# Optimization experiments

Hardware: AMD Instinct MI355X
Metric: run time of the kernel (lower is better)

The kernel has to match this reference:

```python
import jax, jax.numpy as jnp
import numpy as np

B, N, C, T = 2048, 512, 64, 128  # batch, codebook size, latent channels, latent time


def setup_inputs() -> dict:
    key = jax.random.key(0)
    k1, k2 = jax.random.split(key)
    y = jax.random.normal(k1, (B, C, T), dtype=jnp.float32)   # encoder latents
    m = jax.random.normal(k2, (N, C, T), dtype=jnp.float32)   # centroid means
    sd = jnp.ones((N, C, T), dtype=jnp.float32)               # centroid variances
    p = jnp.zeros((N,), dtype=jnp.float32) + 1e-6             # cluster counts
    return {"y": y, "m": m, "sd": sd, "p": p}


def reference(y, m, sd, p):
    # --- squared-distance argmin assignment (same math as (y-m)^2 summed over C,T) ---
    b = y.shape[0]
    yf = y.reshape(b, -1)                 # [B, D]
    mf = m.reshape(m.shape[0], -1)        # [N, D]
    d2 = (yf * yf).sum(-1)[:, None] + (mf * mf).sum(-1)[None, :] - 2.0 * (yf @ mf.T)
    assign = jnp.argmin(d2, axis=1)       # [B] int assignments

    # --- sequential, order-sensitive EMA scatter updates (faithful to python loop) ---
    def step(carry, inp):
        p_, m_, sd_ = carry
        yi, zi = inp
        p_ = p_.at[zi].add(1.0)
        mi = m_[zi] * 0.001 + yi * 0.999
        m_ = m_.at[zi].set(mi)
        sdi = (mi - yi) ** 2 * 0.001 + sd_[zi] * 0.999
        sd_ = sd_.at[zi].set(sdi)
        return (p_, m_, sd_), None

    (p, m, sd), _ = jax.lax.scan(step, (p, m, sd), (y, assign))
    return m, sd, p, assign
```

## Files before the change

kernel.cpp:

```cpp
#include <hip/hip_runtime.h>
#include <hip/hip_bf16.h>


#define Bb 2048
#define Nn 512
#define Dd 8192
#define MARGIN 12.0f
#define KC 8
#define KSTEPS 32

typedef __attribute__((ext_vector_type(4))) float f32x4;
typedef __attribute__((ext_vector_type(8))) short s16x8;

union Frag { unsigned u[4]; s16x8 s; };

__device__ inline unsigned pack2(float lo, float hi) {
    return __builtin_amdgcn_perm(__float_as_uint(hi), __float_as_uint(lo), 0x07060302u);
}

__device__ inline void ema4(float4& mcv, float4& scv, const float4 yv) {
#define EMA_C(c) { mcv.c = mcv.c * 0.001f + yv.c * 0.999f; \
                   float d_ = mcv.c - yv.c;                 \
                   scv.c = d_ * d_ * 0.001f + scv.c * 0.999f; }
    EMA_C(x) EMA_C(y) EMA_C(z) EMA_C(w)
#undef EMA_C
}

__global__ __launch_bounds__(256) void m_norms(const float* __restrict__ M,
                                               float* __restrict__ mm) {
    int n = blockIdx.x, t = threadIdx.x;
    const float4* r = (const float4*)(M + (size_t)n * Dd);
    float s = 0.f;
#pragma unroll
    for (int u = 0; u < 8; u++) {
        float4 v = r[t + 256 * u];
        s += v.x * v.x + v.y * v.y + v.z * v.z + v.w * v.w;
    }
    __shared__ float red[256];
    red[t] = s;
    __syncthreads();
    for (int off = 128; off > 0; off >>= 1) {
        if (t < off) red[t] += red[t + off];
        __syncthreads();
    }
    if (t == 0) mm[n] = red[0];
}

__global__ __launch_bounds__(512, 4) void gemm_coarse(const float* __restrict__ Y,
                                                      const float* __restrict__ M,
                                                      float* __restrict__ part) {
    __shared__ __align__(16) float As[2][128 * 32];
    __shared__ __align__(16) float Bs[2][128 * 32];
    const int t = threadIdx.x;
    const int lane = t & 63;
    const int w = t >> 6;

    const int bid = blockIdx.x;
    const int kc = bid & 7;
    const int ct = (bid >> 3) & 3;
    const int rt = bid >> 5;

    const size_t ybase = (size_t)rt * 128 * Dd + (size_t)kc * (KSTEPS * 32);
    const size_t mbase = (size_t)ct * 128 * Dd + (size_t)kc * (KSTEPS * 32);

    int rowS[2], soff[2];
#pragma unroll
    for (int u = 0; u < 2; u++) {
        int flat = (w * 2 + u) * 64 + lane;
        int row = flat >> 3, seg = flat & 7;
        rowS[u] = row;
        soff[u] = (seg ^ (row & 7)) * 4;
    }

    const int wr0 = (w & 3) * 32, wc0 = (w >> 2) * 64;
    const int l15 = lane & 15, quad = lane >> 4;

    f32x4 acc[2][4];
#pragma unroll
    for (int i = 0; i < 2; i++)
#pragma unroll
        for (int j = 0; j < 4; j++) acc[i][j] = (f32x4)(0.0f);

    auto stage = [&](int buf, int step) {
        const int kpos = step * 32;
#pragma unroll
        for (int u = 0; u < 2; u++) {
            const float* gA = Y + ybase + (size_t)rowS[u] * Dd + kpos + soff[u];
            const float* gB = M + mbase + (size_t)rowS[u] * Dd + kpos + soff[u];
            __builtin_amdgcn_global_load_lds(
                (const __attribute__((address_space(1))) void*)gA,
                (__attribute__((address_space(3))) void*)(&As[buf][0] + (w * 2 + u) * 256), 16, 0, 0);
            __builtin_amdgcn_global_load_lds(
                (const __attribute__((address_space(1))) void*)gB,
                (__attribute__((address_space(3))) void*)(&Bs[buf][0] + (w * 2 + u) * 256), 16, 0, 0);
        }
    };

    auto compute = [&](int buf) {
        Frag fa[2], fb[4];
#pragma unroll
        for (int ta = 0; ta < 2; ta++) {
            int rowa = wr0 + ta * 16 + l15;
            const float* Ar = &As[buf][0] + rowa * 32;
            int s0 = ((quad * 2) ^ (rowa & 7)) * 4;
            int s1 = ((quad * 2 + 1) ^ (rowa & 7)) * 4;
            f32x4 x0 = *(const f32x4*)(Ar + s0);
            f32x4 x1 = *(const f32x4*)(Ar + s1);
            fa[ta].u[0] = pack2(x0[0], x0[1]);
            fa[ta].u[1] = pack2(x0[2], x0[3]);
            fa[ta].u[2] = pack2(x1[0], x1[1]);
            fa[ta].u[3] = pack2(x1[2], x1[3]);
        }
#pragma unroll
        for (int tb = 0; tb < 4; tb++) {
            int rowb = wc0 + tb * 16 + l15;
            const float* Br = &Bs[buf][0] + rowb * 32;
            int s0 = ((quad * 2) ^ (rowb & 7)) * 4;
            int s1 = ((quad * 2 + 1) ^ (rowb & 7)) * 4;
            f32x4 x0 = *(const f32x4*)(Br + s0);
            f32x4 x1 = *(const f32x4*)(Br + s1);
            fb[tb].u[0] = pack2(x0[0], x0[1]);
            fb[tb].u[1] = pack2(x0[2], x0[3]);
            fb[tb].u[2] = pack2(x1[0], x1[1]);
            fb[tb].u[3] = pack2(x1[2], x1[3]);
        }
#pragma unroll
        for (int i = 0; i < 2; i++)
#pragma unroll
            for (int j = 0; j < 4; j++)
                acc[i][j] = __builtin_amdgcn_mfma_f32_16x16x32_bf16(fa[i].s, fb[j].s, acc[i][j], 0, 0, 0);
    };

    stage(0, 0);
    __syncthreads();
    for (int step = 0; step < KSTEPS; step += 2) {
        stage(1, step + 1);
        compute(0);
        __syncthreads();
        if (step + 2 < KSTEPS) stage(0, step + 2);
        compute(1);
        __syncthreads();
    }

    float* P = part + (size_t)kc * (Bb * Nn);
#pragma unroll
    for (int i = 0; i < 2; i++) {
        int rg = rt * 128 + wr0 + i * 16 + quad * 4;
#pragma unroll
        for (int j = 0; j < 4; j++) {
            int cg = ct * 128 + wc0 + j * 16 + l15;
#pragma unroll
            for (int r = 0; r < 4; r++)
                P[(size_t)(rg + r) * Nn + cg] = acc[i][j][r];
        }
    }
}

__global__ __launch_bounds__(256) void rescore(const float* __restrict__ Y,
                                               const float* __restrict__ M,
                                               const float* __restrict__ part,
                                               const float* __restrict__ mm,
                                               float* __restrict__ assignF) {
    __shared__ float redW[4];
    __shared__ int candList[Nn];
    __shared__ float candD2[Nn];
    __shared__ int candCnt;
    int b = blockIdx.x, t = threadIdx.x, lane = t & 63, w = t >> 6;
    if (t == 0) candCnt = 0;

    int c0 = t, c1 = t + 256;
    float dot0 = 0.f, dot1 = 0.f;
#pragma unroll
    for (int k = 0; k < KC; k++) {
        dot0 += part[(size_t)k * (Bb * Nn) + (size_t)b * Nn + c0];
        dot1 += part[(size_t)k * (Bb * Nn) + (size_t)b * Nn + c1];
    }
    float d0 = mm[c0] - 2.0f * dot0;
    float d1 = mm[c1] - 2.0f * dot1;

    float mn = fminf(d0, d1);
#pragma unroll
    for (int off = 32; off > 0; off >>= 1) mn = fminf(mn, __shfl_xor(mn, off));
    if (lane == 0) redW[w] = mn;
    __syncthreads();
    float thresh = fminf(fminf(redW[0], redW[1]), fminf(redW[2], redW[3])) + MARGIN;

    if (d0 <= thresh) candList[atomicAdd(&candCnt, 1)] = c0;
    if (d1 <= thresh) candList[atomicAdd(&candCnt, 1)] = c1;
    __syncthreads();
    int ncand = candCnt;

    if (ncand == 1) {
        if (t == 0) assignF[b] = (float)candList[0];
        return;
    }

    const float4* yr = (const float4*)(Y + (size_t)b * Dd);
    for (int j = w; j < ncand; j += 4) {
        int c = candList[j];
        const float4* mr = (const float4*)(M + (size_t)c * Dd);
        float p = 0.f;
#pragma unroll 8
        for (int u = 0; u < 32; u++) {
            float4 yv = yr[u * 64 + lane];
            float4 mv = mr[u * 64 + lane];
            p += yv.x * mv.x + yv.y * mv.y + yv.z * mv.z + yv.w * mv.w;
        }
#pragma unroll
        for (int off = 32; off > 0; off >>= 1) p += __shfl_xor(p, off);
        if (lane == 0) candD2[j] = mm[c] - 2.0f * p;
    }
    __syncthreads();

    if (t == 0) {
        float bestV = 3.4e38f;
        int bestI = 0x3fffffff;
        for (int j = 0; j < ncand; j++) {
            float d2e = candD2[j];
            int c = candList[j];
            if (d2e < bestV || (d2e == bestV && c < bestI)) { bestV = d2e; bestI = c; }
        }
        assignF[b] = (float)bestI;
    }
}

__global__ __launch_bounds__(256) void ema_scatter(const float* __restrict__ Y,
                                                   const float* __restrict__ M0,
                                                   const float* __restrict__ SD0,
                                                   const float* __restrict__ P0,
                                                   const float* __restrict__ assignF,
                                                   float* __restrict__ m_out,
                                                   float* __restrict__ sd_out,
                                                   float* __restrict__ p_out) {
    __shared__ int lst[Bb];
    __shared__ int cntSh;
    int n = blockIdx.x, s = blockIdx.y, t = threadIdx.x, lane = t & 63, w = t >> 6;

    if (w == 0) {
        int cnt = 0;
#pragma unroll
        for (int u = 0; u < 32; u++) {
            int zi = (int)assignF[u * 64 + lane];
            unsigned long long mask = __ballot(zi == n);
            if (zi == n) lst[cnt + (int)__popcll(mask & ((1ull << lane) - 1ull))] = u * 64 + lane;
            cnt += (int)__popcll(mask);
        }
        if (lane == 0) {
            cntSh = cnt;
            if (s == 0) p_out[n] = P0[n] + (float)cnt;
        }
    }
    __syncthreads();
    int cnt = cntSh;

    size_t off = (size_t)n * Dd + (size_t)s * 1024;
    float4 mc = *(const float4*)(M0 + off + 4 * t);
    float4 sc = *(const float4*)(SD0 + off + 4 * t);

    int j = 0;
    for (; j + 16 <= cnt; j += 16) {
        float4 yv[16];
#pragma unroll
        for (int q = 0; q < 16; q++)
            yv[q] = *(const float4*)(Y + (size_t)lst[j + q] * Dd + (size_t)s * 1024 + 4 * t);
#pragma unroll
        for (int q = 0; q < 16; q++) ema4(mc, sc, yv[q]);
    }
    for (; j < cnt; j++) {
        float4 yv = *(const float4*)(Y + (size_t)lst[j] * Dd + (size_t)s * 1024 + 4 * t);
        ema4(mc, sc, yv);
    }

    *(float4*)(m_out + off + 4 * t) = mc;
    *(float4*)(sd_out + off + 4 * t) = sc;
}

extern "C" void kernel_launch(void* const* d_in, const int* in_sizes, int n_in,
                              void* d_out, int out_size, void* d_ws, size_t ws_size,
                              hipStream_t stream) {
    const float* y  = (const float*)d_in[0];
    const float* m  = (const float*)d_in[1];
    const float* sd = (const float*)d_in[2];
    const float* p  = (const float*)d_in[3];

    float* out     = (float*)d_out;
    float* m_out   = out;
    float* sd_out  = out + 4194304;
    float* p_out   = out + 8388608;
    float* assignF = out + 8389120;
    float* part    = out;

    m_norms    <<<Nn, 256, 0, stream>>>(m, p_out);
    gemm_coarse<<<dim3(512), 512, 0, stream>>>(y, m, part);
    rescore    <<<Bb, 256, 0, stream>>>(y, m, part, p_out, assignF);
    ema_scatter<<<dim3(Nn, 8), 256, 0, stream>>>(y, m, sd, p, assignF, m_out, sd_out, p_out);
}
```

Before: 218.8 us.

## Stage GEMM tiles as bf16 in LDS and parallelize scatter list build

The coarse GEMM no longer uses async global-to-LDS fp32 copies. Each thread now loads fp32 into registers, packs it to bf16 and writes swizzled bf16 to LDS, so LDS footprint and fragment reads are halved and the per-compute conversion work is removed. The price is register-staged prefetching and a single barrier per k-step. The ema_scatter list build is split across all four waves with a prefix offset in place of one wave scanning alone, and a 4-wide unrolled remainder loop is added for the EMA.

```diff
diff --git a/kernel.cpp b/kernel.cpp
--- a/kernel.cpp
+++ b/kernel.cpp
@@ -12,8 +12,6 @@
 typedef __attribute__((ext_vector_type(4))) float f32x4;
 typedef __attribute__((ext_vector_type(8))) short s16x8;
 
-union Frag { unsigned u[4]; s16x8 s; };
-
 __device__ inline unsigned pack2(float lo, float hi) {
     return __builtin_amdgcn_perm(__float_as_uint(hi), __float_as_uint(lo), 0x07060302u);
 }
@@ -49,8 +47,8 @@
 __global__ __launch_bounds__(512, 4) void gemm_coarse(const float* __restrict__ Y,
                                                       const float* __restrict__ M,
                                                       float* __restrict__ part) {
-    __shared__ __align__(16) float As[2][128 * 32];
-    __shared__ __align__(16) float Bs[2][128 * 32];
+    __shared__ __align__(16) unsigned short As[2][128 * 32];
+    __shared__ __align__(16) unsigned short Bs[2][128 * 32];
     const int t = threadIdx.x;
     const int lane = t & 63;
     const int w = t >> 6;
@@ -63,14 +61,11 @@
     const size_t ybase = (size_t)rt * 128 * Dd + (size_t)kc * (KSTEPS * 32);
     const size_t mbase = (size_t)ct * 128 * Dd + (size_t)kc * (KSTEPS * 32);
 
-    int rowS[2], soff[2];
-#pragma unroll
-    for (int u = 0; u < 2; u++) {
-        int flat = (w * 2 + u) * 64 + lane;
-        int row = flat >> 3, seg = flat & 7;
-        rowS[u] = row;
-        soff[u] = (seg ^ (row & 7)) * 4;
-    }
+    const int rowT = t >> 2;
+    const int segT = t & 3;
+    const int dstOff = rowT * 32 + (segT ^ ((rowT >> 1) & 3)) * 8;
+    const float* gA0 = Y + ybase + (size_t)rowT * Dd + segT * 8;
+    const float* gB0 = M + mbase + (size_t)rowT * Dd + segT * 8;
 
     const int wr0 = (w & 3) * 32, wc0 = (w >> 2) * 64;
     const int l15 = lane & 15, quad = lane >> 4;
@@ -81,64 +76,51 @@
 #pragma unroll
         for (int j = 0; j < 4; j++) acc[i][j] = (f32x4)(0.0f);
 
-    auto stage = [&](int buf, int step) {
-        const int kpos = step * 32;
-#pragma unroll
-        for (int u = 0; u < 2; u++) {
-            const float* gA = Y + ybase + (size_t)rowS[u] * Dd + kpos + soff[u];
-            const float* gB = M + mbase + (size_t)rowS[u] * Dd + kpos + soff[u];
-            __builtin_amdgcn_global_load_lds(
-                (const __attribute__((address_space(1))) void*)gA,
-                (__attribute__((address_space(3))) void*)(&As[buf][0] + (w * 2 + u) * 256), 16, 0, 0);
-            __builtin_amdgcn_global_load_lds(
-                (const __attribute__((address_space(1))) void*)gB,
-                (__attribute__((address_space(3))) void*)(&Bs[buf][0] + (w * 2 + u) * 256), 16, 0, 0);
-        }
+    float4 ra0, ra1, rb0, rb1;
+    auto loads = [&](int step) {
+        const float* pa = gA0 + step * 32;
+        const float* pb = gB0 + step * 32;
+        ra0 = *(const float4*)pa;  ra1 = *(const float4*)(pa + 4);
+        rb0 = *(const float4*)pb;  rb1 = *(const float4*)(pb + 4);
     };
-
+    auto writes = [&](int buf) {
+        union { unsigned u[4]; s16x8 s; } pa_, pb_;
+        pa_.u[0] = pack2(ra0.x, ra0.y);  pa_.u[1] = pack2(ra0.z, ra0.w);
+        pa_.u[2] = pack2(ra1.x, ra1.y);  pa_.u[3] = pack2(ra1.z, ra1.w);
+        pb_.u[0] = pack2(rb0.x, rb0.y);  pb_.u[1] = pack2(rb0.z, rb0.w);
+        pb_.u[2] = pack2(rb1.x, rb1.y);  pb_.u[3] = pack2(rb1.z, rb1.w);
+        *(s16x8*)(&As[buf][dstOff]) = pa_.s;
+        *(s16x8*)(&Bs[buf][dstOff]) = pb_.s;
+    };
     auto compute = [&](int buf) {
-        Frag fa[2], fb[4];
+        s16x8 fa[2], fb[4];
 #pragma unroll
         for (int ta = 0; ta < 2; ta++) {
             int rowa = wr0 + ta * 16 + l15;
-            const float* Ar = &As[buf][0] + rowa * 32;
-            int s0 = ((quad * 2) ^ (rowa & 7)) * 4;
-            int s1 = ((quad * 2 + 1) ^ (rowa & 7)) * 4;
-            f32x4 x0 = *(const f32x4*)(Ar + s0);
-            f32x4 x1 = *(const f32x4*)(Ar + s1);
-            fa[ta].u[0] = pack2(x0[0], x0[1]);
-            fa[ta].u[1] = pack2(x0[2], x0[3]);
-            fa[ta].u[2] = pack2(x1[0], x1[1]);
-            fa[ta].u[3] = pack2(x1[2], x1[3]);
+            int sega = quad ^ ((rowa >> 1) & 3);
+            fa[ta] = *(const s16x8*)(&As[buf][rowa * 32 + sega * 8]);
         }
 #pragma unroll
         for (int tb = 0; tb < 4; tb++) {
             int rowb = wc0 + tb * 16 + l15;
-            const float* Br = &Bs[buf][0] + rowb * 32;
-            int s0 = ((quad * 2) ^ (rowb & 7)) * 4;
-            int s1 = ((quad * 2 + 1) ^ (rowb & 7)) * 4;
-            f32x4 x0 = *(const f32x4*)(Br + s0);
-            f32x4 x1 = *(const f32x4*)(Br + s1);
-            fb[tb].u[0] = pack2(x0[0], x0[1]);
-            fb[tb].u[1] = pack2(x0[2], x0[3]);
-            fb[tb].u[2] = pack2(x1[0], x1[1]);
-            fb[tb].u[3] = pack2(x1[2], x1[3]);
+            int segb = quad ^ ((rowb >> 1) & 3);
+            fb[tb] = *(const s16x8*)(&Bs[buf][rowb * 32 + segb * 8]);
         }
 #pragma unroll
         for (int i = 0; i < 2; i++)
 #pragma unroll
             for (int j = 0; j < 4; j++)
-                acc[i][j] = __builtin_amdgcn_mfma_f32_16x16x32_bf16(fa[i].s, fb[j].s, acc[i][j], 0, 0, 0);
+                acc[i][j] = __builtin_amdgcn_mfma_f32_16x16x32_bf16(fa[i], fb[j], acc[i][j], 0, 0, 0);
     };
 
-    stage(0, 0);
-    __syncthreads();
-    for (int step = 0; step < KSTEPS; step += 2) {
-        stage(1, step + 1);
-        compute(0);
-        __syncthreads();
-        if (step + 2 < KSTEPS) stage(0, step + 2);
-        compute(1);
+    loads(0);
+    writes(0);
+    __syncthreads();
+    for (int step = 0; step < KSTEPS; step++) {
+        const int buf = step & 1;
+        if (step + 1 < KSTEPS) loads(step + 1);
+        compute(buf);
+        if (step + 1 < KSTEPS) writes(buf ^ 1);
         __syncthreads();
     }
 
@@ -233,25 +215,32 @@
                                                    float* __restrict__ sd_out,
                                                    float* __restrict__ p_out) {
     __shared__ int lst[Bb];
-    __shared__ int cntSh;
+    __shared__ int cnt4[4];
     int n = blockIdx.x, s = blockIdx.y, t = threadIdx.x, lane = t & 63, w = t >> 6;
 
-    if (w == 0) {
-        int cnt = 0;
-#pragma unroll
-        for (int u = 0; u < 32; u++) {
-            int zi = (int)assignF[u * 64 + lane];
-            unsigned long long mask = __ballot(zi == n);
-            if (zi == n) lst[cnt + (int)__popcll(mask & ((1ull << lane) - 1ull))] = u * 64 + lane;
-            cnt += (int)__popcll(mask);
-        }
-        if (lane == 0) {
-            cntSh = cnt;
-            if (s == 0) p_out[n] = P0[n] + (float)cnt;
-        }
-    }
-    __syncthreads();
-    int cnt = cntSh;
+    int eqf[8], myidx[8];
+    int cntW = 0;
+#pragma unroll
+    for (int k = 0; k < 8; k++) {
+        int u = w * 8 + k;
+        int zi = (int)assignF[u * 64 + lane];
+        int eq = (zi == n) ? 1 : 0;
+        unsigned long long mask = __ballot(eq != 0);
+        eqf[k] = eq;
+        myidx[k] = cntW + (int)__popcll(mask & ((1ull << lane) - 1ull));
+        cntW += (int)__popcll(mask);
+    }
+    if (lane == 0) cnt4[w] = cntW;
+    __syncthreads();
+    int off0 = 0;
+#pragma unroll
+    for (int q = 0; q < 4; q++) off0 += (q < w) ? cnt4[q] : 0;
+    int cnt = cnt4[0] + cnt4[1] + cnt4[2] + cnt4[3];
+#pragma unroll
+    for (int k = 0; k < 8; k++)
+        if (eqf[k]) lst[off0 + myidx[k]] = (w * 8 + k) * 64 + lane;
+    if (t == 0 && s == 0) p_out[n] = P0[n] + (float)cnt;
+    __syncthreads();
 
     size_t off = (size_t)n * Dd + (size_t)s * 1024;
     float4 mc = *(const float4*)(M0 + off + 4 * t);
@@ -265,6 +254,14 @@
             yv[q] = *(const float4*)(Y + (size_t)lst[j + q] * Dd + (size_t)s * 1024 + 4 * t);
 #pragma unroll
         for (int q = 0; q < 16; q++) ema4(mc, sc, yv[q]);
+    }
+    for (; j + 4 <= cnt; j += 4) {
+        float4 yv[4];
+#pragma unroll
+        for (int q = 0; q < 4; q++)
+            yv[q] = *(const float4*)(Y + (size_t)lst[j + q] * Dd + (size_t)s * 1024 + 4 * t);
+#pragma unroll
+        for (int q = 0; q < 4; q++) ema4(mc, sc, yv[q]);
     }
     for (; j < cnt; j++) {
         float4 yv = *(const float4*)(Y + (size_t)lst[j] * Dd + (size_t)s * 1024 + 4 * t);
```

New measurement: 209.4 us. 4.3% less time.
